# Optimization experiments

Hardware: AMD Instinct MI355X
Metric: run time of the kernel (lower is better)

The kernel has to match this reference:

```python
import jax, jax.numpy as jnp
import numpy as np

TOP_K = 2  # config.num_experts_per_tok


def quick_gelu(x):
    return x * jax.nn.sigmoid(1.702 * x)


def setup_inputs() -> dict:
    key = jax.random.key(0)
    ks = jax.random.split(key, 6)
    B, S, H, I, E = 8, 4096, 512, 1024, 8
    s_h = 1.0 / np.sqrt(H).astype(np.float32)
    s_i = 1.0 / np.sqrt(I).astype(np.float32)
    return {
        "hidden_states": jax.random.normal(ks[0], (B, S, H), jnp.float32),
        "router_w": jax.random.normal(ks[1], (H, E), jnp.float32) * s_h,
        "router_b": jnp.zeros((E,), jnp.float32),
        "gate_up_proj": jax.random.normal(ks[2], (E, H, 2 * I), jnp.float32) * s_h,
        "gate_up_proj_bias": jnp.zeros((E, 2 * I), jnp.float32),
        "down_proj": jax.random.normal(ks[3], (E, I, H), jnp.float32) * s_i,
        "down_proj_bias": jnp.zeros((E, H), jnp.float32),
    }


def reference(hidden_states, router_w, router_b, gate_up_proj,
              gate_up_proj_bias, down_proj, down_proj_bias):
    B, S, H = hidden_states.shape
    E = router_b.shape[0]
    x = hidden_states.reshape(-1, H)          # [T, H]
    T = x.shape[0]

    # Router: top-k logits then softmax over the selected k
    logits = x @ router_w + router_b          # [T, E]
    top_w, sel = jax.lax.top_k(logits, TOP_K)  # [T, k]
    top_w = jax.nn.softmax(top_w, axis=-1)

    # Per-token per-expert combine weight (0 for unselected experts) [T, E]
    tok_w = jnp.zeros((T, E), x.dtype).at[jnp.arange(T)[:, None], sel].add(top_w)

    # Loop over the (small, fixed) expert axis; zero weights kill non-routed
    # tokens' contributions, matching the masked gather/scatter exactly.
    def body(acc, params):
        Wgu, bgu, Wd, bd, w_e = params        # w_e: [T]
        gu = x @ Wgu + bgu                    # [T, 2I]
        gate, up = jnp.split(gu, 2, axis=-1)
        act = (up + 1.0) * quick_gelu(gate)   # [T, I]
        out = act @ Wd + bd                   # [T, H]
        return acc + out * w_e[:, None], None

    acc0 = jnp.zeros((T, H), x.dtype)
    acc, _ = jax.lax.scan(
        body, acc0,
        (gate_up_proj, gate_up_proj_bias, down_proj, down_proj_bias, tok_w.T))
    return acc.reshape(B, S, H)
```

## Files before the change

### kernel.cpp

```cpp
#include <hip/hip_runtime.h>

#define T_TOK 32768
#define HDIM  512
#define IDIM  1024
#define NEXP  8
#define BM    64
#define KI    128

typedef float    f32x4 __attribute__((ext_vector_type(4)));
typedef _Float16 f16x8 __attribute__((ext_vector_type(8)));
typedef _Float16 f16x4 __attribute__((ext_vector_type(4)));

__global__ __launch_bounds__(256) void router_kernel(
    const float* __restrict__ x, const float* __restrict__ rw,
    const float* __restrict__ rb, int* __restrict__ cnt,
    int* __restrict__ btok, float* __restrict__ bw)
{
    __shared__ float Wl[HDIM * NEXP];
    __shared__ float xc[64 * 133];
    __shared__ float part[4 * 64 * 8];
    __shared__ int   bcnt[NEXP];
    __shared__ int   sbase[NEXP];

    const int tid = threadIdx.x;
    const int t0  = blockIdx.x * 64;

    if (tid < NEXP) bcnt[tid] = 0;

    for (int j = tid; j < HDIM * NEXP / 4; j += 256)
        ((float4*)Wl)[j] = ((const float4*)rw)[j];

    const int tl = tid & 63;
    const int q  = tid >> 6;

    float acc[8];
#pragma unroll
    for (int e = 0; e < 8; ++e) acc[e] = 0.f;

    for (int hc = 0; hc < 4; ++hc) {
        __syncthreads();
        for (int j = tid; j < 64 * 128 / 4; j += 256) {
            int row = j >> 5;
            int col = (j & 31) * 4;
            float4 v = *(const float4*)(x + (size_t)(t0 + row) * HDIM + hc * 128 + col);
            float* d = &xc[row * 133 + col];
            d[0] = v.x; d[1] = v.y; d[2] = v.z; d[3] = v.w;
        }
        __syncthreads();
#pragma unroll
        for (int hh = 0; hh < 32; ++hh) {
            int h = q * 32 + hh;
            float xv = xc[tl * 133 + h];
            const float* wrow = &Wl[(hc * 128 + h) * 8];
#pragma unroll
            for (int e = 0; e < 8; ++e) acc[e] += xv * wrow[e];
        }
    }
#pragma unroll
    for (int e = 0; e < 8; ++e) part[(q * 64 + tl) * 8 + e] = acc[e];
    __syncthreads();

    int e0 = 0, e1 = 0, l0 = 0, l1 = 0;
    float w0 = 0.f, w1 = 0.f;
    if (tid < 64) {
        float lg[8];
#pragma unroll
        for (int e = 0; e < 8; ++e)
            lg[e] = part[(0 * 64 + tid) * 8 + e] + part[(1 * 64 + tid) * 8 + e] +
                    part[(2 * 64 + tid) * 8 + e] + part[(3 * 64 + tid) * 8 + e] + rb[e];
#pragma unroll
        for (int e = 1; e < 8; ++e) if (lg[e] > lg[e0]) e0 = e;
        e1 = (e0 == 0) ? 1 : 0;
#pragma unroll
        for (int e = 0; e < 8; ++e) if (e != e0 && lg[e] > lg[e1]) e1 = e;
        float z = __expf(lg[e1] - lg[e0]);
        w0 = 1.f / (1.f + z);
        w1 = z * w0;
        l0 = atomicAdd(&bcnt[e0], 1);
        l1 = atomicAdd(&bcnt[e1], 1);
    }
    __syncthreads();
    if (tid < NEXP) sbase[tid] = atomicAdd(&cnt[tid], bcnt[tid]);
    __syncthreads();
    if (tid < 64) {
        int t  = t0 + tid;
        int s0 = sbase[e0] + l0;
        btok[e0 * T_TOK + s0] = t;  bw[e0 * T_TOK + s0] = w0;
        int s1 = sbase[e1] + l1;
        btok[e1 * T_TOK + s1] = t;  bw[e1 * T_TOK + s1] = w1;
    }
}

template <int R, int C>
__global__ __launch_bounds__(256) void transpose_cvt(
    const float* __restrict__ src, _Float16* __restrict__ dst)
{
    __shared__ float tile[32][33];
    const int e  = blockIdx.z;
    const int rb = blockIdx.y * 32, cb = blockIdx.x * 32;
    const int t  = threadIdx.x;
    {
        const int lr = t >> 3, lc = (t & 7) * 4;
        float4 v = *(const float4*)(src + ((size_t)e * R + rb + lr) * C + cb + lc);
        tile[lr][lc + 0] = v.x; tile[lr][lc + 1] = v.y;
        tile[lr][lc + 2] = v.z; tile[lr][lc + 3] = v.w;
    }
    __syncthreads();
    {
        const int c = t >> 3, r4 = (t & 7) * 4;
        f16x4 h;
        h[0] = (_Float16)tile[r4 + 0][c];
        h[1] = (_Float16)tile[r4 + 1][c];
        h[2] = (_Float16)tile[r4 + 2][c];
        h[3] = (_Float16)tile[r4 + 3][c];
        *(f16x4*)(dst + ((size_t)e * C + cb + c) * R + rb + r4) = h;
    }
}

__global__ __launch_bounds__(512) void moe_kernel(
    const float* __restrict__ x,
    const _Float16* __restrict__ wgu_t,
    const float* __restrict__ bgu,
    const _Float16* __restrict__ wd_t,
    const float* __restrict__ bd,
    const int* __restrict__ cnt,
    const int* __restrict__ btok,
    const float* __restrict__ bw,
    float* __restrict__ out)
{
    const int bid = blockIdx.x;
    const int e   = bid & 7;
    const int m0  = (bid >> 3) * BM;
    const int n_e = cnt[e];
    if (m0 >= n_e) return;

    __shared__ __align__(16) _Float16 A[BM * HDIM];
    __shared__ __align__(16) _Float16 ACT[2][BM * KI];
    __shared__ int   s_tok[BM];
    __shared__ float s_w[BM];

    const int tid  = threadIdx.x;
    const int lane = tid & 63;
    const int wv   = tid >> 6;
    const int bn   = lane & 15;
    const int bk   = (lane >> 4) * 8;

    if (tid < BM) {
        int idx = m0 + tid;
        if (idx < n_e) { s_tok[tid] = btok[e * T_TOK + idx]; s_w[tid] = bw[e * T_TOK + idx]; }
        else           { s_tok[tid] = -1;                    s_w[tid] = 0.f; }
    }
    __syncthreads();

    {
        const int r  = tid >> 3;
        const int tk = s_tok[r];
#pragma unroll
        for (int j = 0; j < 8; ++j) {
            const int c = ((tid & 7) + j * 8) * 8;
            float4 f0, f1;
            if (tk >= 0) {
                const float4* p = (const float4*)(x + (size_t)tk * HDIM + c);
                f0 = p[0]; f1 = p[1];
            } else { f0 = make_float4(0, 0, 0, 0); f1 = f0; }
            f16x8 h;
            h[0] = (_Float16)f0.x; h[1] = (_Float16)f0.y;
            h[2] = (_Float16)f0.z; h[3] = (_Float16)f0.w;
            h[4] = (_Float16)f1.x; h[5] = (_Float16)f1.y;
            h[6] = (_Float16)f1.z; h[7] = (_Float16)f1.w;
            int byte = r * 1024 + c * 2;  byte ^= (r & 7) << 4;
            *(f16x8*)((char*)A + byte) = h;
        }
    }
    __syncthreads();

    f32x4 accO[4][4];
#pragma unroll
    for (int mt = 0; mt < 4; ++mt)
#pragma unroll
        for (int nt = 0; nt < 4; ++nt)
#pragma unroll
            for (int r = 0; r < 4; ++r) accO[mt][nt][r] = 0.f;

    for (int ic = 0; ic < IDIM / KI; ++ic) {
        char* actb = (char*)ACT + (ic & 1) * (BM * KI * 2);

        f32x4 accG[4], accU[4];
#pragma unroll
        for (int mt = 0; mt < 4; ++mt)
#pragma unroll
            for (int r = 0; r < 4; ++r) { accG[mt][r] = 0.f; accU[mt][r] = 0.f; }

        const _Float16* bg = wgu_t + ((size_t)(e * 2 * IDIM) + ic * KI + wv * 16 + bn) * HDIM;
        const _Float16* bu = bg + (size_t)IDIM * HDIM;

#pragma unroll
        for (int ks = 0; ks < 16; ++ks) {
            const int k0 = ks * 32 + bk;
            f16x8 bgf = *(const f16x8*)(bg + k0);
            f16x8 buf = *(const f16x8*)(bu + k0);
#pragma unroll
            for (int mt = 0; mt < 4; ++mt) {
                const int m = mt * 16 + bn;
                int byte = m * 1024 + k0 * 2;  byte ^= (m & 7) << 4;
                f16x8 af = *(const f16x8*)((const char*)A + byte);
                accG[mt] = __builtin_amdgcn_mfma_f32_16x16x32_f16(af, bgf, accG[mt], 0, 0, 0);
                accU[mt] = __builtin_amdgcn_mfma_f32_16x16x32_f16(af, buf, accU[mt], 0, 0, 0);
            }
        }
        const int   gidx = e * 2 * IDIM + ic * KI + wv * 16 + bn;
        const float bgv  = bgu[gidx];
        const float buv  = bgu[gidx + IDIM];
#pragma unroll
        for (int mt = 0; mt < 4; ++mt) {
#pragma unroll
            for (int r = 0; r < 4; ++r) {
                float g = accG[mt][r] + bgv;
                float u = accU[mt][r] + buv;
                float a = (u + 1.f) * g / (1.f + __expf(-1.702f * g));
                const int row = mt * 16 + ((lane >> 4) << 2) + r;
                const int col = wv * 16 + bn;
                int byte = row * 256 + col * 2;  byte ^= (row & 7) << 4;
                *(_Float16*)(actb + byte) = (_Float16)a;
            }
        }
        __syncthreads();

        const _Float16* bdp = wd_t + ((size_t)(e * HDIM) + wv * 64) * IDIM;
#pragma unroll
        for (int ks = 0; ks < 4; ++ks) {
            const int kl = ks * 32 + bk;
            const int kg = ic * KI + kl;
            f16x8 bf[4];
#pragma unroll
            for (int nt = 0; nt < 4; ++nt)
                bf[nt] = *(const f16x8*)(bdp + (size_t)(nt * 16 + bn) * IDIM + kg);
#pragma unroll
            for (int mt = 0; mt < 4; ++mt) {
                const int m = mt * 16 + bn;
                int byte = m * 256 + kl * 2;  byte ^= (m & 7) << 4;
                f16x8 af = *(const f16x8*)((const char*)actb + byte);
#pragma unroll
                for (int nt = 0; nt < 4; ++nt)
                    accO[mt][nt] = __builtin_amdgcn_mfma_f32_16x16x32_f16(af, bf[nt], accO[mt][nt], 0, 0, 0);
            }
        }
    }

    float bdv[4];
#pragma unroll
    for (int nt = 0; nt < 4; ++nt) bdv[nt] = bd[e * HDIM + wv * 64 + nt * 16 + bn];
#pragma unroll
    for (int mt = 0; mt < 4; ++mt) {
#pragma unroll
        for (int r = 0; r < 4; ++r) {
            const int m  = mt * 16 + ((lane >> 4) << 2) + r;
            const int tk = s_tok[m];
            if (tk < 0) continue;
            const float wgt = s_w[m];
            float* orow = out + (size_t)tk * HDIM + wv * 64 + bn;
#pragma unroll
            for (int nt = 0; nt < 4; ++nt)
                atomicAdd(orow + nt * 16, (accO[mt][nt][r] + bdv[nt]) * wgt);
        }
    }
}

extern "C" void kernel_launch(void* const* d_in, const int* in_sizes, int n_in,
                              void* d_out, int out_size, void* d_ws, size_t ws_size,
                              hipStream_t stream)
{
    const float* x   = (const float*)d_in[0];
    const float* rw  = (const float*)d_in[1];
    const float* rb  = (const float*)d_in[2];
    const float* wgu = (const float*)d_in[3];
    const float* bgu = (const float*)d_in[4];
    const float* wd  = (const float*)d_in[5];
    const float* bd  = (const float*)d_in[6];
    float* out = (float*)d_out;

    char* ws = (char*)d_ws;
    size_t o = 0;
    int*   cnt  = (int*)(ws + o);   o += 256;
    int*   btok = (int*)(ws + o);   o += (size_t)NEXP * T_TOK * 4;
    float* bwp  = (float*)(ws + o); o += (size_t)NEXP * T_TOK * 4;
    _Float16* wgu_t = (_Float16*)(ws + o); o += (size_t)NEXP * 2 * IDIM * HDIM * 2;
    _Float16* wd_t  = (_Float16*)(ws + o); o += (size_t)NEXP * HDIM * IDIM * 2;

    hipMemsetAsync(cnt, 0, 256, stream);
    hipMemsetAsync(out, 0, (size_t)out_size * 4, stream);

    transpose_cvt<HDIM, 2 * IDIM><<<dim3(2 * IDIM / 32, HDIM / 32, NEXP), 256, 0, stream>>>(wgu, wgu_t);
    transpose_cvt<IDIM, HDIM><<<dim3(HDIM / 32, IDIM / 32, NEXP), 256, 0, stream>>>(wd, wd_t);
    router_kernel<<<T_TOK / 64, 256, 0, stream>>>(x, rw, rb, cnt, btok, bwp);
    moe_kernel<<<dim3((T_TOK / BM) * NEXP), 512, 0, stream>>>(
        x, wgu_t, bgu, wd_t, bd, cnt, btok, bwp, out);
}
```

Measured before the change: 773.4 us.

## Stage gate/up weights through double-buffered LDS with async global_load_lds

```diff
diff --git a/kernel.cpp b/kernel.cpp
--- a/kernel.cpp
+++ b/kernel.cpp
@@ -10,6 +10,11 @@
 typedef float    f32x4 __attribute__((ext_vector_type(4)));
 typedef _Float16 f16x8 __attribute__((ext_vector_type(8)));
 typedef _Float16 f16x4 __attribute__((ext_vector_type(4)));
+
+#define GL2LDS(gp, lp)                                                        \
+    __builtin_amdgcn_global_load_lds(                                         \
+        (const __attribute__((address_space(1))) void*)(gp),                  \
+        (__attribute__((address_space(3))) void*)(lp), 16, 0, 0)
 
 __global__ __launch_bounds__(256) void router_kernel(
     const float* __restrict__ x, const float* __restrict__ rw,
@@ -135,6 +140,7 @@
     if (m0 >= n_e) return;
 
     __shared__ __align__(16) _Float16 A[BM * HDIM];
+    __shared__ __align__(16) _Float16 BGU[2 * 8192];
     __shared__ __align__(16) _Float16 ACT[2][BM * KI];
     __shared__ int   s_tok[BM];
     __shared__ float s_w[BM];
@@ -145,12 +151,25 @@
     const int bn   = lane & 15;
     const int bk   = (lane >> 4) * 8;
 
+    const int d1 = tid * 16;
+    const int u1 = d1 ^ (((d1 >> 7) & 7) << 4);
+    const int d2 = d1 + 8192;
+    const int u2 = d2 ^ (((d2 >> 7) & 7) << 4);
+    const _Float16* wguE = wgu_t + (size_t)e * 2 * IDIM * HDIM;
+    const _Float16* sp1  = wguE + ((size_t)(((u1 >> 6) & 1) * IDIM + (u1 >> 7))) * HDIM + ((u1 & 63) >> 1);
+    const _Float16* sp2  = wguE + ((size_t)(((u2 >> 6) & 1) * IDIM + (u2 >> 7))) * HDIM + ((u2 & 63) >> 1);
+    _Float16* lp1 = BGU + tid * 8;
+    _Float16* lp2 = lp1 + 4096;
+
     if (tid < BM) {
         int idx = m0 + tid;
         if (idx < n_e) { s_tok[tid] = btok[e * T_TOK + idx]; s_w[tid] = bw[e * T_TOK + idx]; }
         else           { s_tok[tid] = -1;                    s_w[tid] = 0.f; }
     }
     __syncthreads();
+
+    GL2LDS(sp1, lp1);
+    GL2LDS(sp2, lp2);
 
     {
         const int r  = tid >> 3;
@@ -172,7 +191,6 @@
             *(f16x8*)((char*)A + byte) = h;
         }
     }
-    __syncthreads();
 
     f32x4 accO[4][4];
 #pragma unroll
@@ -182,33 +200,50 @@
 #pragma unroll
             for (int r = 0; r < 4; ++r) accO[mt][nt][r] = 0.f;
 
+    const int colu = wv * 16 + bn;
+    const int sw   = (colu & 7) << 4;
+    const int bgOff = colu * 128 + ((bk * 2) ^ sw);
+    const int buOff = colu * 128 + ((64 + bk * 2) ^ sw);
+
     for (int ic = 0; ic < IDIM / KI; ++ic) {
-        char* actb = (char*)ACT + (ic & 1) * (BM * KI * 2);
-
         f32x4 accG[4], accU[4];
 #pragma unroll
         for (int mt = 0; mt < 4; ++mt)
 #pragma unroll
             for (int r = 0; r < 4; ++r) { accG[mt][r] = 0.f; accU[mt][r] = 0.f; }
 
-        const _Float16* bg = wgu_t + ((size_t)(e * 2 * IDIM) + ic * KI + wv * 16 + bn) * HDIM;
-        const _Float16* bu = bg + (size_t)IDIM * HDIM;
-
-#pragma unroll
         for (int ks = 0; ks < 16; ++ks) {
-            const int k0 = ks * 32 + bk;
-            f16x8 bgf = *(const f16x8*)(bg + k0);
-            f16x8 buf = *(const f16x8*)(bu + k0);
+            __syncthreads();
+            if (ks < 15) {
+                const _Float16* q1 = sp1 + (size_t)ic * KI * HDIM + (ks + 1) * 32;
+                const _Float16* q2 = sp2 + (size_t)ic * KI * HDIM + (ks + 1) * 32;
+                _Float16* t1 = lp1 + ((ks + 1) & 1) * 8192;
+                _Float16* t2 = lp2 + ((ks + 1) & 1) * 8192;
+                GL2LDS(q1, t1);
+                GL2LDS(q2, t2);
+            } else if (ic < IDIM / KI - 1) {
+                const _Float16* q1 = sp1 + (size_t)(ic + 1) * KI * HDIM;
+                const _Float16* q2 = sp2 + (size_t)(ic + 1) * KI * HDIM;
+                GL2LDS(q1, lp1);
+                GL2LDS(q2, lp2);
+            }
+
+            const char* bb = (const char*)BGU + (ks & 1) * 16384;
+            f16x8 bgf = *(const f16x8*)(bb + bgOff);
+            f16x8 buf_ = *(const f16x8*)(bb + buOff);
+            const int k0b = (ks * 32 + bk) * 2;
 #pragma unroll
             for (int mt = 0; mt < 4; ++mt) {
                 const int m = mt * 16 + bn;
-                int byte = m * 1024 + k0 * 2;  byte ^= (m & 7) << 4;
+                int byte = m * 1024 + k0b;  byte ^= (m & 7) << 4;
                 f16x8 af = *(const f16x8*)((const char*)A + byte);
                 accG[mt] = __builtin_amdgcn_mfma_f32_16x16x32_f16(af, bgf, accG[mt], 0, 0, 0);
-                accU[mt] = __builtin_amdgcn_mfma_f32_16x16x32_f16(af, buf, accU[mt], 0, 0, 0);
+                accU[mt] = __builtin_amdgcn_mfma_f32_16x16x32_f16(af, buf_, accU[mt], 0, 0, 0);
             }
         }
-        const int   gidx = e * 2 * IDIM + ic * KI + wv * 16 + bn;
+
+        char* actb = (char*)ACT + (ic & 1) * (BM * KI * 2);
+        const int   gidx = e * 2 * IDIM + ic * KI + colu;
         const float bgv  = bgu[gidx];
         const float buv  = bgu[gidx + IDIM];
 #pragma unroll
@@ -219,8 +254,7 @@
                 float u = accU[mt][r] + buv;
                 float a = (u + 1.f) * g / (1.f + __expf(-1.702f * g));
                 const int row = mt * 16 + ((lane >> 4) << 2) + r;
-                const int col = wv * 16 + bn;
-                int byte = row * 256 + col * 2;  byte ^= (row & 7) << 4;
+                int byte = row * 256 + colu * 2;  byte ^= (row & 7) << 4;
                 *(_Float16*)(actb + byte) = (_Float16)a;
             }
         }
```

Measured after the change: 748.2 us. 3.3% less time.

## Split fused MoE kernel into chunked gate-up and down GEMMs with padded expert layout

Applied to the files above, without the earlier changes.

```diff
diff --git a/kernel.cpp b/kernel.cpp
--- a/kernel.cpp
+++ b/kernel.cpp
@@ -4,12 +4,17 @@
 #define HDIM  512
 #define IDIM  1024
 #define NEXP  8
-#define BM    64
-#define KI    128
+#define CHUNK 16384
+#define NCHUNK 5
 
 typedef float    f32x4 __attribute__((ext_vector_type(4)));
 typedef _Float16 f16x8 __attribute__((ext_vector_type(8)));
 typedef _Float16 f16x4 __attribute__((ext_vector_type(4)));
+
+#define GL2LDS(gp, lp)                                                        \
+    __builtin_amdgcn_global_load_lds(                                         \
+        (const __attribute__((address_space(1))) void*)(gp),                  \
+        (__attribute__((address_space(3))) void*)(lp), 16, 0, 0)
 
 __global__ __launch_bounds__(256) void router_kernel(
     const float* __restrict__ x, const float* __restrict__ rw,
@@ -117,151 +122,272 @@
     }
 }
 
-__global__ __launch_bounds__(512) void moe_kernel(
+__global__ void prefix_kernel(const int* __restrict__ cnt, int* __restrict__ eb)
+{
+    if (threadIdx.x == 0 && blockIdx.x == 0) {
+        int a = 0;
+#pragma unroll
+        for (int e = 0; e < 8; ++e) { eb[e] = a; a += (cnt[e] + 127) & ~127; }
+        eb[8] = a;
+    }
+}
+
+__global__ __launch_bounds__(256) void repack_kernel(
+    const int* __restrict__ cnt, const int* __restrict__ eb,
+    const int* __restrict__ btok, const float* __restrict__ bw,
+    int* __restrict__ btok_p, float* __restrict__ bw_p)
+{
+    const int e = blockIdx.y;
+    const int i = blockIdx.x * 256 + threadIdx.x;
+    const int span = eb[e + 1] - eb[e];
+    if (i >= span) return;
+    const int c = cnt[e];
+    const int p = eb[e] + i;
+    if (i < c) { btok_p[p] = btok[e * T_TOK + i]; bw_p[p] = bw[e * T_TOK + i]; }
+    else       { btok_p[p] = (c > 0) ? btok[e * T_TOK] : 0; bw_p[p] = 0.f; }
+}
+
+__global__ __launch_bounds__(256) void k1_gateup(
     const float* __restrict__ x,
     const _Float16* __restrict__ wgu_t,
     const float* __restrict__ bgu,
+    const int* __restrict__ eb,
+    const int* __restrict__ btok_p,
+    _Float16* __restrict__ act,
+    int chunk)
+{
+    const int gs0 = chunk * CHUNK + blockIdx.x * 128;
+    if (gs0 >= eb[8]) return;
+    int e = 0;
+#pragma unroll
+    for (int k = 1; k < 8; ++k) if (eb[k] <= gs0) e = k;
+    const int n0 = blockIdx.y * 64;
+
+    __shared__ __align__(16) _Float16 Ab[2][128 * 32];
+    __shared__ __align__(16) _Float16 Bg[2][64 * 32];
+    __shared__ __align__(16) _Float16 Bu[2][64 * 32];
+    __shared__ int s_tok[128];
+
+    const int tid  = threadIdx.x;
+    const int lane = tid & 63;
+    const int w    = tid >> 6;
+    const int wm   = w >> 1, wn = w & 1;
+    const int bn   = lane & 15;
+    const int bq   = lane >> 4;
+    const int bk2  = bq * 16;
+
+    if (tid < 128) s_tok[tid] = btok_p[gs0 + tid];
+    __syncthreads();
+
+    const int ar = tid >> 1;
+    const int ah = tid & 1;
+    const float* axp = x + (size_t)s_tok[ar] * HDIM + ah * 16;
+    const int ab0 = ar * 64 + ((ah * 32)      ^ ((ar & 3) << 4));
+    const int ab1 = ar * 64 + ((ah * 32 + 16) ^ ((ar & 3) << 4));
+
+    const int rl = lane >> 2, ch = lane & 3;
+    const _Float16* bsg = wgu_t + ((size_t)e * 2 * IDIM + n0 + w * 16 + rl) * HDIM
+                          + (ch ^ (rl & 3)) * 8;
+    const _Float16* bsu = bsg + (size_t)IDIM * HDIM;
+    _Float16* dg0 = &Bg[0][w * 512] + lane * 8;
+    _Float16* du0 = &Bu[0][w * 512] + lane * 8;
+    _Float16* dg1 = &Bg[1][w * 512] + lane * 8;
+    _Float16* du1 = &Bu[1][w * 512] + lane * 8;
+
+    f32x4 aG[4][2], aU[4][2];
+#pragma unroll
+    for (int mt = 0; mt < 4; ++mt)
+#pragma unroll
+        for (int nt = 0; nt < 2; ++nt)
+#pragma unroll
+            for (int r = 0; r < 4; ++r) { aG[mt][nt][r] = 0.f; aU[mt][nt][r] = 0.f; }
+
+    {
+        const float4* p = (const float4*)axp;
+        float4 v0 = p[0], v1 = p[1], v2 = p[2], v3 = p[3];
+        f16x8 h0, h1;
+        h0[0]=(_Float16)v0.x; h0[1]=(_Float16)v0.y; h0[2]=(_Float16)v0.z; h0[3]=(_Float16)v0.w;
+        h0[4]=(_Float16)v1.x; h0[5]=(_Float16)v1.y; h0[6]=(_Float16)v1.z; h0[7]=(_Float16)v1.w;
+        h1[0]=(_Float16)v2.x; h1[1]=(_Float16)v2.y; h1[2]=(_Float16)v2.z; h1[3]=(_Float16)v2.w;
+        h1[4]=(_Float16)v3.x; h1[5]=(_Float16)v3.y; h1[6]=(_Float16)v3.z; h1[7]=(_Float16)v3.w;
+        *(f16x8*)((char*)Ab[0] + ab0) = h0;
+        *(f16x8*)((char*)Ab[0] + ab1) = h1;
+        GL2LDS(bsg, dg0);
+        GL2LDS(bsu, du0);
+    }
+    __syncthreads();
+
+    for (int ks = 0; ks < 16; ++ks) {
+        const int cur = ks & 1;
+        float4 v0, v1, v2, v3;
+        if (ks < 15) {
+            const float4* p = (const float4*)(axp + (ks + 1) * 32);
+            v0 = p[0]; v1 = p[1]; v2 = p[2]; v3 = p[3];
+            GL2LDS(bsg + (ks + 1) * 32, cur ? dg0 : dg1);
+            GL2LDS(bsu + (ks + 1) * 32, cur ? du0 : du1);
+        }
+
+        const char* ab = (const char*)Ab[cur];
+        const char* gb = (const char*)Bg[cur];
+        const char* ub = (const char*)Bu[cur];
+        f16x8 bgf[2], buf_[2];
+#pragma unroll
+        for (int nt = 0; nt < 2; ++nt) {
+            const int j = wn * 32 + nt * 16 + bn;
+            const int byte = j * 64 + (bk2 ^ ((j & 3) << 4));
+            bgf[nt]  = *(const f16x8*)(gb + byte);
+            buf_[nt] = *(const f16x8*)(ub + byte);
+        }
+#pragma unroll
+        for (int mt = 0; mt < 4; ++mt) {
+            const int m = wm * 64 + mt * 16 + bn;
+            const int byte = m * 64 + (bk2 ^ ((m & 3) << 4));
+            f16x8 af = *(const f16x8*)(ab + byte);
+            aG[mt][0] = __builtin_amdgcn_mfma_f32_16x16x32_f16(af, bgf[0],  aG[mt][0], 0, 0, 0);
+            aG[mt][1] = __builtin_amdgcn_mfma_f32_16x16x32_f16(af, bgf[1],  aG[mt][1], 0, 0, 0);
+            aU[mt][0] = __builtin_amdgcn_mfma_f32_16x16x32_f16(af, buf_[0], aU[mt][0], 0, 0, 0);
+            aU[mt][1] = __builtin_amdgcn_mfma_f32_16x16x32_f16(af, buf_[1], aU[mt][1], 0, 0, 0);
+        }
+
+        if (ks < 15) {
+            f16x8 h0, h1;
+            h0[0]=(_Float16)v0.x; h0[1]=(_Float16)v0.y; h0[2]=(_Float16)v0.z; h0[3]=(_Float16)v0.w;
+            h0[4]=(_Float16)v1.x; h0[5]=(_Float16)v1.y; h0[6]=(_Float16)v1.z; h0[7]=(_Float16)v1.w;
+            h1[0]=(_Float16)v2.x; h1[1]=(_Float16)v2.y; h1[2]=(_Float16)v2.z; h1[3]=(_Float16)v2.w;
+            h1[4]=(_Float16)v3.x; h1[5]=(_Float16)v3.y; h1[6]=(_Float16)v3.z; h1[7]=(_Float16)v3.w;
+            char* an = (char*)Ab[cur ^ 1];
+            *(f16x8*)(an + ab0) = h0;
+            *(f16x8*)(an + ab1) = h1;
+        }
+        __syncthreads();
+    }
+
+    float gB[2], uB[2];
+    int jcol[2];
+#pragma unroll
+    for (int nt = 0; nt < 2; ++nt) {
+        jcol[nt] = n0 + wn * 32 + nt * 16 + bn;
+        gB[nt] = bgu[e * 2 * IDIM + jcol[nt]];
+        uB[nt] = bgu[e * 2 * IDIM + IDIM + jcol[nt]];
+    }
+#pragma unroll
+    for (int mt = 0; mt < 4; ++mt) {
+#pragma unroll
+        for (int r = 0; r < 4; ++r) {
+            const int rr = wm * 64 + mt * 16 + bq * 4 + r;
+            _Float16* arow = act + (size_t)(blockIdx.x * 128 + rr) * IDIM;
+#pragma unroll
+            for (int nt = 0; nt < 2; ++nt) {
+                float g = aG[mt][nt][r] + gB[nt];
+                float u = aU[mt][nt][r] + uB[nt];
+                float a = (u + 1.f) * g / (1.f + __expf(-1.702f * g));
+                arow[jcol[nt]] = (_Float16)a;
+            }
+        }
+    }
+}
+
+__global__ __launch_bounds__(256) void k2_down(
+    const _Float16* __restrict__ act,
     const _Float16* __restrict__ wd_t,
     const float* __restrict__ bd,
-    const int* __restrict__ cnt,
-    const int* __restrict__ btok,
-    const float* __restrict__ bw,
-    float* __restrict__ out)
-{
-    const int bid = blockIdx.x;
-    const int e   = bid & 7;
-    const int m0  = (bid >> 3) * BM;
-    const int n_e = cnt[e];
-    if (m0 >= n_e) return;
-
-    __shared__ __align__(16) _Float16 A[BM * HDIM];
-    __shared__ __align__(16) _Float16 ACT[2][BM * KI];
-    __shared__ int   s_tok[BM];
-    __shared__ float s_w[BM];
+    const int* __restrict__ eb,
+    const int* __restrict__ btok_p,
+    const float* __restrict__ bw_p,
+    float* __restrict__ out, int chunk)
+{
+    const int gs0 = chunk * CHUNK + blockIdx.x * 128;
+    if (gs0 >= eb[8]) return;
+    int e = 0;
+#pragma unroll
+    for (int k = 1; k < 8; ++k) if (eb[k] <= gs0) e = k;
+    const int h0 = blockIdx.y * 128;
+
+    __shared__ __align__(16) _Float16 Ab[2][128 * 32];
+    __shared__ __align__(16) _Float16 Bb[2][128 * 32];
+    __shared__ int   s_tok[128];
+    __shared__ float s_w[128];
 
     const int tid  = threadIdx.x;
     const int lane = tid & 63;
-    const int wv   = tid >> 6;
+    const int w    = tid >> 6;
+    const int wm   = w >> 1, wn = w & 1;
     const int bn   = lane & 15;
-    const int bk   = (lane >> 4) * 8;
-
-    if (tid < BM) {
-        int idx = m0 + tid;
-        if (idx < n_e) { s_tok[tid] = btok[e * T_TOK + idx]; s_w[tid] = bw[e * T_TOK + idx]; }
-        else           { s_tok[tid] = -1;                    s_w[tid] = 0.f; }
-    }
-    __syncthreads();
-
-    {
-        const int r  = tid >> 3;
-        const int tk = s_tok[r];
-#pragma unroll
-        for (int j = 0; j < 8; ++j) {
-            const int c = ((tid & 7) + j * 8) * 8;
-            float4 f0, f1;
-            if (tk >= 0) {
-                const float4* p = (const float4*)(x + (size_t)tk * HDIM + c);
-                f0 = p[0]; f1 = p[1];
-            } else { f0 = make_float4(0, 0, 0, 0); f1 = f0; }
-            f16x8 h;
-            h[0] = (_Float16)f0.x; h[1] = (_Float16)f0.y;
-            h[2] = (_Float16)f0.z; h[3] = (_Float16)f0.w;
-            h[4] = (_Float16)f1.x; h[5] = (_Float16)f1.y;
-            h[6] = (_Float16)f1.z; h[7] = (_Float16)f1.w;
-            int byte = r * 1024 + c * 2;  byte ^= (r & 7) << 4;
-            *(f16x8*)((char*)A + byte) = h;
-        }
-    }
-    __syncthreads();
-
-    f32x4 accO[4][4];
+    const int bq   = lane >> 4;
+    const int bk2  = bq * 16;
+
+    if (tid < 128) { s_tok[tid] = btok_p[gs0 + tid]; s_w[tid] = bw_p[gs0 + tid]; }
+
+    const int rl = lane >> 2, ch = lane & 3;
+    const int swz8 = (ch ^ (rl & 3)) * 8;
+    const _Float16* as0 = act + (size_t)(blockIdx.x * 128 + w * 32 + rl) * IDIM + swz8;
+    const _Float16* as1 = as0 + (size_t)16 * IDIM;
+    const _Float16* bs0 = wd_t + ((size_t)e * HDIM + h0 + w * 32 + rl) * IDIM + swz8;
+    const _Float16* bs1 = bs0 + (size_t)16 * IDIM;
+
+    f32x4 acc[4][4];
 #pragma unroll
     for (int mt = 0; mt < 4; ++mt)
 #pragma unroll
         for (int nt = 0; nt < 4; ++nt)
 #pragma unroll
-            for (int r = 0; r < 4; ++r) accO[mt][nt][r] = 0.f;
-
-    for (int ic = 0; ic < IDIM / KI; ++ic) {
-        char* actb = (char*)ACT + (ic & 1) * (BM * KI * 2);
-
-        f32x4 accG[4], accU[4];
-#pragma unroll
-        for (int mt = 0; mt < 4; ++mt)
-#pragma unroll
-            for (int r = 0; r < 4; ++r) { accG[mt][r] = 0.f; accU[mt][r] = 0.f; }
-
-        const _Float16* bg = wgu_t + ((size_t)(e * 2 * IDIM) + ic * KI + wv * 16 + bn) * HDIM;
-        const _Float16* bu = bg + (size_t)IDIM * HDIM;
-
-#pragma unroll
-        for (int ks = 0; ks < 16; ++ks) {
-            const int k0 = ks * 32 + bk;
-            f16x8 bgf = *(const f16x8*)(bg + k0);
-            f16x8 buf = *(const f16x8*)(bu + k0);
-#pragma unroll
-            for (int mt = 0; mt < 4; ++mt) {
-                const int m = mt * 16 + bn;
-                int byte = m * 1024 + k0 * 2;  byte ^= (m & 7) << 4;
-                f16x8 af = *(const f16x8*)((const char*)A + byte);
-                accG[mt] = __builtin_amdgcn_mfma_f32_16x16x32_f16(af, bgf, accG[mt], 0, 0, 0);
-                accU[mt] = __builtin_amdgcn_mfma_f32_16x16x32_f16(af, buf, accU[mt], 0, 0, 0);
-            }
-        }
-        const int   gidx = e * 2 * IDIM + ic * KI + wv * 16 + bn;
-        const float bgv  = bgu[gidx];
-        const float buv  = bgu[gidx + IDIM];
+            for (int r = 0; r < 4; ++r) acc[mt][nt][r] = 0.f;
+
+    GL2LDS(as0, &Ab[0][w * 1024] + lane * 8);
+    GL2LDS(as1, &Ab[0][w * 1024 + 512] + lane * 8);
+    GL2LDS(bs0, &Bb[0][w * 1024] + lane * 8);
+    GL2LDS(bs1, &Bb[0][w * 1024 + 512] + lane * 8);
+    __syncthreads();
+
+    for (int ks = 0; ks < 32; ++ks) {
+        const int cur = ks & 1;
+        if (ks < 31) {
+            const int ko = (ks + 1) * 32;
+            _Float16* a0 = &Ab[cur ^ 1][w * 1024] + lane * 8;
+            _Float16* b0 = &Bb[cur ^ 1][w * 1024] + lane * 8;
+            GL2LDS(as0 + ko, a0);
+            GL2LDS(as1 + ko, a0 + 512);
+            GL2LDS(bs0 + ko, b0);
+            GL2LDS(bs1 + ko, b0 + 512);
+        }
+
+        const char* ab = (const char*)Ab[cur];
+        const char* bb = (const char*)Bb[cur];
+        f16x8 bf[4];
+#pragma unroll
+        for (int nt = 0; nt < 4; ++nt) {
+            const int n = wn * 64 + nt * 16 + bn;
+            bf[nt] = *(const f16x8*)(bb + n * 64 + (bk2 ^ ((n & 3) << 4)));
+        }
 #pragma unroll
         for (int mt = 0; mt < 4; ++mt) {
-#pragma unroll
-            for (int r = 0; r < 4; ++r) {
-                float g = accG[mt][r] + bgv;
-                float u = accU[mt][r] + buv;
-                float a = (u + 1.f) * g / (1.f + __expf(-1.702f * g));
-                const int row = mt * 16 + ((lane >> 4) << 2) + r;
-                const int col = wv * 16 + bn;
-                int byte = row * 256 + col * 2;  byte ^= (row & 7) << 4;
-                *(_Float16*)(actb + byte) = (_Float16)a;
-            }
+            const int m = wm * 64 + mt * 16 + bn;
+            f16x8 af = *(const f16x8*)(ab + m * 64 + (bk2 ^ ((m & 3) << 4)));
+#pragma unroll
+            for (int nt = 0; nt < 4; ++nt)
+                acc[mt][nt] = __builtin_amdgcn_mfma_f32_16x16x32_f16(af, bf[nt], acc[mt][nt], 0, 0, 0);
         }
         __syncthreads();
-
-        const _Float16* bdp = wd_t + ((size_t)(e * HDIM) + wv * 64) * IDIM;
-#pragma unroll
-        for (int ks = 0; ks < 4; ++ks) {
-            const int kl = ks * 32 + bk;
-            const int kg = ic * KI + kl;
-            f16x8 bf[4];
+    }
+
+    float bdv[4];
+    int   col[4];
+#pragma unroll
+    for (int nt = 0; nt < 4; ++nt) {
+        col[nt] = h0 + wn * 64 + nt * 16 + bn;
+        bdv[nt] = bd[e * HDIM + col[nt]];
+    }
+#pragma unroll
+    for (int mt = 0; mt < 4; ++mt) {
+#pragma unroll
+        for (int r = 0; r < 4; ++r) {
+            const int rr = wm * 64 + mt * 16 + bq * 4 + r;
+            const float wt = s_w[rr];
+            if (wt == 0.f) continue;
+            float* orow = out + (size_t)s_tok[rr] * HDIM;
 #pragma unroll
             for (int nt = 0; nt < 4; ++nt)
-                bf[nt] = *(const f16x8*)(bdp + (size_t)(nt * 16 + bn) * IDIM + kg);
-#pragma unroll
-            for (int mt = 0; mt < 4; ++mt) {
-                const int m = mt * 16 + bn;
-                int byte = m * 256 + kl * 2;  byte ^= (m & 7) << 4;
-                f16x8 af = *(const f16x8*)((const char*)actb + byte);
-#pragma unroll
-                for (int nt = 0; nt < 4; ++nt)
-                    accO[mt][nt] = __builtin_amdgcn_mfma_f32_16x16x32_f16(af, bf[nt], accO[mt][nt], 0, 0, 0);
-            }
-        }
-    }
-
-    float bdv[4];
-#pragma unroll
-    for (int nt = 0; nt < 4; ++nt) bdv[nt] = bd[e * HDIM + wv * 64 + nt * 16 + bn];
-#pragma unroll
-    for (int mt = 0; mt < 4; ++mt) {
-#pragma unroll
-        for (int r = 0; r < 4; ++r) {
-            const int m  = mt * 16 + ((lane >> 4) << 2) + r;
-            const int tk = s_tok[m];
-            if (tk < 0) continue;
-            const float wgt = s_w[m];
-            float* orow = out + (size_t)tk * HDIM + wv * 64 + bn;
-#pragma unroll
-            for (int nt = 0; nt < 4; ++nt)
-                atomicAdd(orow + nt * 16, (accO[mt][nt][r] + bdv[nt]) * wgt);
+                atomicAdd(orow + col[nt], wt * (acc[mt][nt][r] + bdv[nt]));
         }
     }
 }
@@ -281,11 +407,15 @@
 
     char* ws = (char*)d_ws;
     size_t o = 0;
-    int*   cnt  = (int*)(ws + o);   o += 256;
-    int*   btok = (int*)(ws + o);   o += (size_t)NEXP * T_TOK * 4;
-    float* bwp  = (float*)(ws + o); o += (size_t)NEXP * T_TOK * 4;
+    int*   cnt    = (int*)(ws + o);   o += 256;
+    int*   eb     = (int*)(ws + o);   o += 256;
+    int*   btok   = (int*)(ws + o);   o += (size_t)NEXP * T_TOK * 4;
+    float* bwp    = (float*)(ws + o); o += (size_t)NEXP * T_TOK * 4;
+    int*   btok_p = (int*)(ws + o);   o += (size_t)NCHUNK * CHUNK * 4;
+    float* bw_p   = (float*)(ws + o); o += (size_t)NCHUNK * CHUNK * 4;
     _Float16* wgu_t = (_Float16*)(ws + o); o += (size_t)NEXP * 2 * IDIM * HDIM * 2;
     _Float16* wd_t  = (_Float16*)(ws + o); o += (size_t)NEXP * HDIM * IDIM * 2;
+    _Float16* act   = (_Float16*)(ws + o); o += (size_t)CHUNK * IDIM * 2;
 
     hipMemsetAsync(cnt, 0, 256, stream);
     hipMemsetAsync(out, 0, (size_t)out_size * 4, stream);
@@ -293,6 +423,13 @@
     transpose_cvt<HDIM, 2 * IDIM><<<dim3(2 * IDIM / 32, HDIM / 32, NEXP), 256, 0, stream>>>(wgu, wgu_t);
     transpose_cvt<IDIM, HDIM><<<dim3(HDIM / 32, IDIM / 32, NEXP), 256, 0, stream>>>(wd, wd_t);
     router_kernel<<<T_TOK / 64, 256, 0, stream>>>(x, rw, rb, cnt, btok, bwp);
-    moe_kernel<<<dim3((T_TOK / BM) * NEXP), 512, 0, stream>>>(
-        x, wgu_t, bgu, wd_t, bd, cnt, btok, bwp, out);
-}
+    prefix_kernel<<<1, 64, 0, stream>>>(cnt, eb);
+    repack_kernel<<<dim3(T_TOK / 256, NEXP), 256, 0, stream>>>(cnt, eb, btok, bwp, btok_p, bw_p);
+
+    for (int c = 0; c < NCHUNK; ++c) {
+        k1_gateup<<<dim3(CHUNK / 128, IDIM / 64), 256, 0, stream>>>(
+            x, wgu_t, bgu, eb, btok_p, act, c);
+        k2_down<<<dim3(CHUNK / 128, HDIM / 128), 256, 0, stream>>>(
+            act, wd_t, bd, eb, btok_p, bw_p, out, c);
+    }
+}
```

Result: faster. 691.6 us (-10.6%).
